# Performance work log

Measured on AMD Instinct MI355X. Metric: run time of the kernel, lower is better.

Reference implementation:

```python
import jax, jax.numpy as jnp
import numpy as np

EMB = 512
H = 8
D = EMB // H
N_TOK = 2048
IN_EMB = 1024
SCALE = EMB ** 0.5  # note: original divides AFTER softmax
EPS = 1e-5


def _layer_norm(x, g, b):
    m = x.mean(-1, keepdims=True)
    v = ((x - m) ** 2).mean(-1, keepdims=True)
    return (x - m) / jnp.sqrt(v + EPS) * g + b


def _mhla(x, idx, Wq, bq, Wk, bk, Wv, bv):
    # x: [b, n, EMB]; idx: [n, k] int neighbor indices into token axis
    b, n, _ = x.shape
    def heads(y):
        return y.reshape(b, n, H, D).transpose(0, 2, 1, 3)  # b h n d
    q = heads(x @ Wq + bq)
    k = heads(x @ Wk + bk)
    v = heads(x @ Wv + bv)
    Kl = k[:, :, idx, :]  # b h n k d  (gather of local keys)
    Vl = v[:, :, idx, :]  # b h n k d
    energy = jnp.einsum('bhnd,bhnkd->bhnk', q, Kl)
    att = jax.nn.softmax(energy, axis=-1) / SCALE  # faithful: scale after softmax
    patch_att = att.sum(axis=(1, 3)).T  # [n, b] (sum over heads, neighbors; stacked over n)
    out = jnp.einsum('bhnk,bhnkd->bhnd', att, Vl)
    out = out.transpose(0, 2, 1, 3).reshape(b, n, EMB)
    return out, patch_att


def setup_inputs() -> dict:
    key = jax.random.key(0)
    ks = jax.random.split(key, 16)
    def p(k, shape, s=0.02):
        return jax.random.normal(k, shape, dtype=jnp.float32) * s
    inp = {
        'x': jax.random.normal(ks[0], (1, N_TOK, IN_EMB), dtype=jnp.float32),
        'A': jax.random.randint(ks[1], (1, N_TOK, 64), 0, N_TOK),
        'W_fc': p(ks[2], (IN_EMB, EMB)), 'b_fc': jnp.zeros((EMB,), jnp.float32),
        'Wq1': p(ks[3], (EMB, EMB)), 'bq1': jnp.zeros((EMB,), jnp.float32),
        'Wk1': p(ks[4], (EMB, EMB)), 'bk1': jnp.zeros((EMB,), jnp.float32),
        'Wv1': p(ks[5], (EMB, EMB)), 'bv1': jnp.zeros((EMB,), jnp.float32),
        'g1': jnp.ones((EMB,), jnp.float32), 'be1': jnp.zeros((EMB,), jnp.float32),
        'Wq2': p(ks[6], (EMB, EMB)), 'bq2': jnp.zeros((EMB,), jnp.float32),
        'Wk2': p(ks[7], (EMB, EMB)), 'bk2': jnp.zeros((EMB,), jnp.float32),
        'Wv2': p(ks[8], (EMB, EMB)), 'bv2': jnp.zeros((EMB,), jnp.float32),
        'g2': jnp.ones((EMB,), jnp.float32), 'be2': jnp.zeros((EMB,), jnp.float32),
    }
    return inp


def reference(x, A, W_fc, b_fc, Wq1, bq1, Wk1, bk1, Wv1, bv1, g1, be1,
              Wq2, bq2, Wk2, bk2, Wv2, bv2, g2, be2):
    embs = jax.nn.relu(x @ W_fc + b_fc)  # FeedForwardBlock (dropout p=0)
    idx = A[0]  # batch==1 as required by torch.squeeze semantics in original
    b1, _ = _mhla(embs, idx[:, :16], Wq1, bq1, Wk1, bk1, Wv1, bv1)
    b1 = _layer_norm(b1 + embs, g1, be1)
    b2, Att2 = _mhla(b1, idx[:, :64], Wq2, bq2, Wk2, bk2, Wv2, bv2)
    b2 = _layer_norm(b2 + b1, g2, be2)
    return b2, Att2
```

## Files before the change

### kernel.cpp

```cpp
#include <hip/hip_runtime.h>

#define SCALE 22.627416997969522f
#define LNEPS 1e-5f

using short8 = __attribute__((ext_vector_type(8))) short;
using f32x4  = __attribute__((ext_vector_type(4))) float;
typedef unsigned short u16;
using u16x4 = __attribute__((ext_vector_type(4))) u16;

static __device__ __forceinline__ short f2bf(float f){
  unsigned u = __builtin_bit_cast(unsigned, f);
  u += 0x7FFFu + ((u >> 16) & 1u);
  return (short)(u >> 16);
}
static __device__ __forceinline__ float bf2f(u16 u){
  unsigned v = ((unsigned)u) << 16;
  return __builtin_bit_cast(float, v);
}

__global__ __launch_bounds__(256) void cvt_k(const float* __restrict__ src,
                                             u16* __restrict__ dst, int n)
{
  int i = (blockIdx.x * 256 + threadIdx.x) * 4;
  if (i >= n) return;
  float4 v = *(const float4*)(src + i);
  u16x4 o;
  o[0] = (u16)f2bf(v.x); o[1] = (u16)f2bf(v.y);
  o[2] = (u16)f2bf(v.z); o[3] = (u16)f2bf(v.w);
  *(u16x4*)(dst + i) = o;
}

__global__ __launch_bounds__(256) void tr_k(
    const float* __restrict__ W0, const float* __restrict__ W1,
    const float* __restrict__ W2, const float* __restrict__ W3,
    const float* __restrict__ W4, const float* __restrict__ W5,
    u16* __restrict__ T0, u16* __restrict__ T1, u16* __restrict__ T2,
    u16* __restrict__ T3, u16* __restrict__ T4, u16* __restrict__ T5,
    int K, int N)
{
  int z = blockIdx.z;
  const float* W = (z==0)?W0:(z==1)?W1:(z==2)?W2:(z==3)?W3:(z==4)?W4:W5;
  u16*         T = (z==0)?T0:(z==1)?T1:(z==2)?T2:(z==3)?T3:(z==4)?T4:T5;

  __shared__ float tile[32][33];
  int n0 = blockIdx.x * 32, k0 = blockIdx.y * 32;
  int tx = threadIdx.x & 31, ty = threadIdx.x >> 5;
#pragma unroll
  for (int i = 0; i < 32; i += 8)
    tile[ty + i][tx] = W[(size_t)(k0 + ty + i) * N + n0 + tx];
  __syncthreads();
#pragma unroll
  for (int i = 0; i < 32; i += 8)
    T[(size_t)(n0 + ty + i) * K + k0 + tx] = (u16)f2bf(tile[tx][ty + i]);
}

template<bool RELU, bool SPLIT3>
__global__ __launch_bounds__(256) void gemm_k(
    const u16* __restrict__ A, int K,
    const u16* __restrict__ T0, const u16* __restrict__ T1, const u16* __restrict__ T2,
    const float* __restrict__ B0, const float* __restrict__ B1, const float* __restrict__ B2,
    float* __restrict__ C0f, u16* __restrict__ C0b,
    u16* __restrict__ C1, u16* __restrict__ C2)
{
  __shared__ u16 As[64*64];
  __shared__ u16 Bs[64*64];

  int bm = blockIdx.x;
  int nglob = blockIdx.y * 64;
  int sel  = SPLIT3 ? (nglob >> 9) : 0;
  int ncol = nglob & 511;
  const u16*   T  = (sel==0) ? T0 : (sel==1) ? T1 : T2;
  const float* Bv = (sel==0) ? B0 : (sel==1) ? B1 : B2;

  int t = threadIdx.x;
  int wave = t >> 6, lane = t & 63;
  int wm = (wave >> 1) * 32, wn = (wave & 1) * 32;
  int lr = lane & 15, kg = lane >> 4;

  int o0 = t*16, o1 = 4096 + t*16;
  int r0 = o0 >> 7, cb0 = o0 & 127;
  int r1 = o1 >> 7, cb1 = o1 & 127;
  const char* Ag0 = (const char*)(A + (size_t)(bm*64 + r0) * K) + cb0;
  const char* Ag1 = (const char*)(A + (size_t)(bm*64 + r1) * K) + cb1;
  const char* Bg0 = (const char*)(T + (size_t)(ncol  + r0) * K) + cb0;
  const char* Bg1 = (const char*)(T + (size_t)(ncol  + r1) * K) + cb1;
  char* Ad0 = (char*)As + r0*128 + (cb0 ^ ((r0 & 7) << 4));
  char* Ad1 = (char*)As + r1*128 + (cb1 ^ ((r1 & 7) << 4));
  char* Bd0 = (char*)Bs + r0*128 + (cb0 ^ ((r0 & 7) << 4));
  char* Bd1 = (char*)Bs + r1*128 + (cb1 ^ ((r1 & 7) << 4));

  int sw = (lr & 7) << 4;
  const char* Afr0 = (const char*)As + (wm + lr) * 128;
  const char* Afr1 = (const char*)As + (wm + 16 + lr) * 128;
  const char* Bfr0 = (const char*)Bs + (wn + lr) * 128;
  const char* Bfr1 = (const char*)Bs + (wn + 16 + lr) * 128;

  f32x4 acc[2][2] = {};

  short8 pa0 = *(const short8*)Ag0;
  short8 pa1 = *(const short8*)Ag1;
  short8 pb0 = *(const short8*)Bg0;
  short8 pb1 = *(const short8*)Bg1;

  for (int k0 = 0; k0 < K; k0 += 64) {
    __syncthreads();
    *(short8*)Ad0 = pa0;  *(short8*)Ad1 = pa1;
    *(short8*)Bd0 = pb0;  *(short8*)Bd1 = pb1;
    __syncthreads();
    int kn = k0 + 64;
    if (kn < K) {
      pa0 = *(const short8*)(Ag0 + kn*2);
      pa1 = *(const short8*)(Ag1 + kn*2);
      pb0 = *(const short8*)(Bg0 + kn*2);
      pb1 = *(const short8*)(Bg1 + kn*2);
    }
#pragma unroll
    for (int ks = 0; ks < 2; ++ks) {
      int cb = (ks*64 + kg*16) ^ sw;
      short8 af0 = *(const short8*)(Afr0 + cb);
      short8 af1 = *(const short8*)(Afr1 + cb);
      short8 bf0 = *(const short8*)(Bfr0 + cb);
      short8 bf1 = *(const short8*)(Bfr1 + cb);
      acc[0][0] = __builtin_amdgcn_mfma_f32_16x16x32_bf16(af0, bf0, acc[0][0], 0, 0, 0);
      acc[0][1] = __builtin_amdgcn_mfma_f32_16x16x32_bf16(af0, bf1, acc[0][1], 0, 0, 0);
      acc[1][0] = __builtin_amdgcn_mfma_f32_16x16x32_bf16(af1, bf0, acc[1][0], 0, 0, 0);
      acc[1][1] = __builtin_amdgcn_mfma_f32_16x16x32_bf16(af1, bf1, acc[1][1], 0, 0, 0);
    }
  }

#pragma unroll
  for (int mi = 0; mi < 2; ++mi)
#pragma unroll
    for (int ni = 0; ni < 2; ++ni) {
      int col = ncol + wn + ni*16 + lr;
      float bia = Bv[col];
#pragma unroll
      for (int r = 0; r < 4; ++r) {
        int row = bm*64 + wm + mi*16 + kg*4 + r;
        float vv = acc[mi][ni][r] + bia;
        if (RELU) vv = fmaxf(vv, 0.f);
        if (SPLIT3) {
          u16* C = (sel==0) ? C0b : (sel==1) ? C1 : C2;
          C[(size_t)row*512 + col] = (u16)f2bf(vv);
        } else {
          C0f[(size_t)row*512 + col] = vv;
          C0b[(size_t)row*512 + col] = (u16)f2bf(vv);
        }
      }
    }
}

template<int KLOC>
__global__ __launch_bounds__(256) void attn_k(
    const u16* __restrict__ Qb, const u16* __restrict__ Kb, const u16* __restrict__ Vb,
    const int* __restrict__ Aidx,
    const float* __restrict__ resid,
    const float* __restrict__ gma, const float* __restrict__ bta,
    float* __restrict__ outp, u16* __restrict__ outb, float* __restrict__ attOut)
{
  __shared__ float q_s[512];
  __shared__ float att_s[8*KLOC];
  __shared__ float o_s[512];
  __shared__ int   idx_s[KLOC];
  __shared__ float red_s[8];

  int n = blockIdx.x;
  int t = threadIdx.x, w = t >> 6, lane = t & 63;

  q_s[t]       = bf2f(Qb[(size_t)n*512 + t]);
  q_s[t + 256] = bf2f(Qb[(size_t)n*512 + t + 256]);
  if (t < KLOC) idx_s[t] = Aidx[(size_t)n*64 + t];
  __syncthreads();

  if (KLOC == 64) {
    int idx = idx_s[lane];
    int h0 = w*2, h1 = h0 + 1;
    const u16* kp = Kb + (size_t)idx*512;
    float e0 = 0.f, e1 = 0.f;
#pragma unroll
    for (int d0 = 0; d0 < 64; d0 += 8) {
      short8 k0 = *(const short8*)(kp + h0*64 + d0);
      short8 k1 = *(const short8*)(kp + h1*64 + d0);
#pragma unroll
      for (int i = 0; i < 8; ++i) {
        e0 = fmaf(q_s[h0*64 + d0 + i], bf2f((u16)k0[i]), e0);
        e1 = fmaf(q_s[h1*64 + d0 + i], bf2f((u16)k1[i]), e1);
      }
    }
#pragma unroll
    for (int hh = 0; hh < 2; ++hh) {
      float e = hh ? e1 : e0;
      float m = e;
      m = fmaxf(m, __shfl_xor(m, 1));  m = fmaxf(m, __shfl_xor(m, 2));
      m = fmaxf(m, __shfl_xor(m, 4));  m = fmaxf(m, __shfl_xor(m, 8));
      m = fmaxf(m, __shfl_xor(m, 16)); m = fmaxf(m, __shfl_xor(m, 32));
      float p = __expf(e - m);
      float s = p;
      s += __shfl_xor(s, 1);  s += __shfl_xor(s, 2);  s += __shfl_xor(s, 4);
      s += __shfl_xor(s, 8);  s += __shfl_xor(s, 16); s += __shfl_xor(s, 32);
      att_s[(h0 + hh)*64 + lane] = p / (s * SCALE);
    }
  } else {
    int h  = w*2 + (lane >> 5);
    int j  = lane & 15;
    int dh = (lane >> 4) & 1;
    int idx = idx_s[j];
    const u16*   kp = Kb + (size_t)idx*512 + h*64 + dh*32;
    const float* qp = q_s + h*64 + dh*32;
    float e = 0.f;
#pragma unroll
    for (int d0 = 0; d0 < 32; d0 += 8) {
      short8 kk = *(const short8*)(kp + d0);
#pragma unroll
      for (int i = 0; i < 8; ++i)
        e = fmaf(qp[d0 + i], bf2f((u16)kk[i]), e);
    }
    e += __shfl_xor(e, 16);
    float m = e;
    m = fmaxf(m, __shfl_xor(m, 1)); m = fmaxf(m, __shfl_xor(m, 2));
    m = fmaxf(m, __shfl_xor(m, 4)); m = fmaxf(m, __shfl_xor(m, 8));
    float p = __expf(e - m);
    float s = p;
    s += __shfl_xor(s, 1); s += __shfl_xor(s, 2);
    s += __shfl_xor(s, 4); s += __shfl_xor(s, 8);
    att_s[h*16 + j] = p / (s * SCALE);
  }
  __syncthreads();

  {
    int jg = lane >> 3, dc = lane & 7;
#pragma unroll
    for (int hh = 0; hh < 2; ++hh) {
      int h = w*2 + hh;
      float vacc[8] = {0.f,0.f,0.f,0.f,0.f,0.f,0.f,0.f};
#pragma unroll
      for (int jb = 0; jb < KLOC; jb += 8) {
        int j = jb + jg;
        const u16* vp = Vb + (size_t)idx_s[j]*512 + h*64 + dc*8;
        short8 vv = *(const short8*)vp;
        float a = att_s[h*KLOC + j];
#pragma unroll
        for (int i = 0; i < 8; ++i)
          vacc[i] = fmaf(a, bf2f((u16)vv[i]), vacc[i]);
      }
#pragma unroll
      for (int i = 0; i < 8; ++i) {
        vacc[i] += __shfl_xor(vacc[i], 8);
        vacc[i] += __shfl_xor(vacc[i], 16);
        vacc[i] += __shfl_xor(vacc[i], 32);
      }
      if (jg == 0) {
#pragma unroll
        for (int i = 0; i < 8; ++i)
          o_s[h*64 + dc*8 + i] = vacc[i];
      }
    }
  }
  __syncthreads();

  float x0 = o_s[t]       + __builtin_nontemporal_load(resid + (size_t)n*512 + t);
  float x1 = o_s[t + 256] + __builtin_nontemporal_load(resid + (size_t)n*512 + t + 256);
  float s  = x0 + x1, ss = x0*x0 + x1*x1;
  s += __shfl_xor(s, 1);  ss += __shfl_xor(ss, 1);
  s += __shfl_xor(s, 2);  ss += __shfl_xor(ss, 2);
  s += __shfl_xor(s, 4);  ss += __shfl_xor(ss, 4);
  s += __shfl_xor(s, 8);  ss += __shfl_xor(ss, 8);
  s += __shfl_xor(s, 16); ss += __shfl_xor(ss, 16);
  s += __shfl_xor(s, 32); ss += __shfl_xor(ss, 32);
  if (lane == 0) { red_s[w] = s; red_s[4 + w] = ss; }
  __syncthreads();
  float tot  = red_s[0] + red_s[1] + red_s[2] + red_s[3];
  float tots = red_s[4] + red_s[5] + red_s[6] + red_s[7];
  float mean = tot  * (1.0f/512.0f);
  float var  = tots * (1.0f/512.0f) - mean*mean;
  float rstd = rsqrtf(var + LNEPS);
  float y0 = (x0 - mean)*rstd*gma[t]       + bta[t];
  float y1 = (x1 - mean)*rstd*gma[t + 256] + bta[t + 256];
  __builtin_nontemporal_store(y0, outp + (size_t)n*512 + t);
  __builtin_nontemporal_store(y1, outp + (size_t)n*512 + t + 256);
  if (outb != nullptr) {
    outb[(size_t)n*512 + t]       = (u16)f2bf(y0);
    outb[(size_t)n*512 + t + 256] = (u16)f2bf(y1);
  }
  if (attOut != nullptr && t == 0) attOut[n] = 8.0f / SCALE;
}

extern "C" void kernel_launch(void* const* d_in, const int* in_sizes, int n_in,
                              void* d_out, int out_size, void* d_ws, size_t ws_size,
                              hipStream_t stream)
{
  const float* x   = (const float*)d_in[0];
  const int*   A   = (const int*)  d_in[1];
  const float* Wfc = (const float*)d_in[2];
  const float* bfc = (const float*)d_in[3];
  const float* Wq1 = (const float*)d_in[4];
  const float* bq1 = (const float*)d_in[5];
  const float* Wk1 = (const float*)d_in[6];
  const float* bk1 = (const float*)d_in[7];
  const float* Wv1 = (const float*)d_in[8];
  const float* bv1 = (const float*)d_in[9];
  const float* g1  = (const float*)d_in[10];
  const float* be1 = (const float*)d_in[11];
  const float* Wq2 = (const float*)d_in[12];
  const float* bq2 = (const float*)d_in[13];
  const float* Wk2 = (const float*)d_in[14];
  const float* bk2 = (const float*)d_in[15];
  const float* Wv2 = (const float*)d_in[16];
  const float* bv2 = (const float*)d_in[17];
  const float* g2  = (const float*)d_in[18];
  const float* be2 = (const float*)d_in[19];

  char* ws = (char*)d_ws;
  const size_t SZ = (size_t)2048*512;
  float* embs = (float*)ws;                    ws += SZ*4;
  float* b1   = (float*)ws;                    ws += SZ*4;
  u16* embs_b = (u16*)ws;                      ws += SZ*2;
  u16* b1_b   = (u16*)ws;                      ws += SZ*2;
  u16* qb     = (u16*)ws;                      ws += SZ*2;
  u16* kb     = (u16*)ws;                      ws += SZ*2;
  u16* vb     = (u16*)ws;                      ws += SZ*2;
  u16* xb     = (u16*)ws;                      ws += (size_t)2048*1024*2;
  u16* t_fc   = (u16*)ws;                      ws += (size_t)512*1024*2;
  u16* t_q1   = (u16*)ws;                      ws += (size_t)512*512*2;
  u16* t_k1   = (u16*)ws;                      ws += (size_t)512*512*2;
  u16* t_v1   = (u16*)ws;                      ws += (size_t)512*512*2;
  u16* t_q2   = (u16*)ws;                      ws += (size_t)512*512*2;
  u16* t_k2   = (u16*)ws;                      ws += (size_t)512*512*2;
  u16* t_v2   = (u16*)ws;                      ws += (size_t)512*512*2;

  float* out  = (float*)d_out;
  float* att2 = out + SZ;

  dim3 blk(256);
  cvt_k<<<dim3(2048), blk, 0, stream>>>(x, xb, 2048*1024);
  tr_k<<<dim3(16, 32, 1), blk, 0, stream>>>(Wfc, Wfc, Wfc, Wfc, Wfc, Wfc,
      t_fc, t_fc, t_fc, t_fc, t_fc, t_fc, 1024, 512);
  tr_k<<<dim3(16, 16, 6), blk, 0, stream>>>(Wq1, Wk1, Wv1, Wq2, Wk2, Wv2,
      t_q1, t_k1, t_v1, t_q2, t_k2, t_v2, 512, 512);

  gemm_k<true,false><<<dim3(32, 8), blk, 0, stream>>>(xb, 1024,
      t_fc, nullptr, nullptr, bfc, nullptr, nullptr, embs, embs_b, nullptr, nullptr);
  gemm_k<false,true><<<dim3(32, 24), blk, 0, stream>>>(embs_b, 512,
      t_q1, t_k1, t_v1, bq1, bk1, bv1, nullptr, qb, kb, vb);
  attn_k<16><<<dim3(2048), blk, 0, stream>>>(qb, kb, vb, A, embs, g1, be1, b1, b1_b, nullptr);
  gemm_k<false,true><<<dim3(32, 24), blk, 0, stream>>>(b1_b, 512,
      t_q2, t_k2, t_v2, bq2, bk2, bv2, nullptr, qb, kb, vb);
  attn_k<64><<<dim3(2048), blk, 0, stream>>>(qb, kb, vb, A, b1, g2, be2, out, nullptr, att2);
}
```

Before: 188.1 us.

## Stage gathered K and V rows in swizzled shared memory before attention math

Each block now loads its gathered neighbor K rows into an XOR-swizzled LDS buffer with coalesced full-row loads, computes energies from LDS, then reuses the same buffer for V rows before the weighted sum. This replaces scattered per-lane global reads with row-contiguous loads and swizzled LDS accesses that avoid bank conflicts. The Q load is also vectorized to two elements per thread. The cost is 64KB of LDS for the 64-neighbor kernel, which limits occupancy to very few blocks per CU, plus two extra barriers.

```diff
diff --git a/kernel.cpp b/kernel.cpp
--- a/kernel.cpp
+++ b/kernel.cpp
@@ -158,6 +158,7 @@
     const float* __restrict__ gma, const float* __restrict__ bta,
     float* __restrict__ outp, u16* __restrict__ outb, float* __restrict__ attOut)
 {
+  __shared__ u16   kv_s[KLOC*512];
   __shared__ float q_s[512];
   __shared__ float att_s[8*KLOC];
   __shared__ float o_s[512];
@@ -167,24 +168,37 @@
   int n = blockIdx.x;
   int t = threadIdx.x, w = t >> 6, lane = t & 63;
 
-  q_s[t]       = bf2f(Qb[(size_t)n*512 + t]);
-  q_s[t + 256] = bf2f(Qb[(size_t)n*512 + t + 256]);
+  {
+    ushort2 qv = *(const ushort2*)(Qb + (size_t)n*512 + 2*t);
+    q_s[2*t]   = bf2f(qv.x);
+    q_s[2*t+1] = bf2f(qv.y);
+  }
   if (t < KLOC) idx_s[t] = Aidx[(size_t)n*64 + t];
   __syncthreads();
 
+  constexpr int RPW = KLOC/4;
+#pragma unroll
+  for (int jj = 0; jj < RPW; ++jj) {
+    int j = w*RPW + jj;
+    short8 vv = ((const short8*)(Kb + (size_t)idx_s[j]*512))[lane];
+    *(short8*)((char*)kv_s + j*1024 + ((lane*16) ^ ((j&7)<<4))) = vv;
+  }
+  __syncthreads();
+
   if (KLOC == 64) {
-    int idx = idx_s[lane];
+    int j = lane;
+    const char* kp = (const char*)kv_s + j*1024;
+    int swz = (j&7) << 4;
     int h0 = w*2, h1 = h0 + 1;
-    const u16* kp = Kb + (size_t)idx*512;
     float e0 = 0.f, e1 = 0.f;
 #pragma unroll
-    for (int d0 = 0; d0 < 64; d0 += 8) {
-      short8 k0 = *(const short8*)(kp + h0*64 + d0);
-      short8 k1 = *(const short8*)(kp + h1*64 + d0);
+    for (int c = 0; c < 8; ++c) {
+      short8 k0 = *(const short8*)(kp + ((h0*128 + c*16) ^ swz));
+      short8 k1 = *(const short8*)(kp + ((h1*128 + c*16) ^ swz));
 #pragma unroll
       for (int i = 0; i < 8; ++i) {
-        e0 = fmaf(q_s[h0*64 + d0 + i], bf2f((u16)k0[i]), e0);
-        e1 = fmaf(q_s[h1*64 + d0 + i], bf2f((u16)k1[i]), e1);
+        e0 = fmaf(q_s[h0*64 + c*8 + i], bf2f((u16)k0[i]), e0);
+        e1 = fmaf(q_s[h1*64 + c*8 + i], bf2f((u16)k1[i]), e1);
       }
     }
 #pragma unroll
@@ -204,16 +218,16 @@
     int h  = w*2 + (lane >> 5);
     int j  = lane & 15;
     int dh = (lane >> 4) & 1;
-    int idx = idx_s[j];
-    const u16*   kp = Kb + (size_t)idx*512 + h*64 + dh*32;
-    const float* qp = q_s + h*64 + dh*32;
+    const char* kp = (const char*)kv_s + j*1024;
+    int swz = (j&7) << 4;
+    int base = h*128 + dh*64;
     float e = 0.f;
 #pragma unroll
-    for (int d0 = 0; d0 < 32; d0 += 8) {
-      short8 kk = *(const short8*)(kp + d0);
+    for (int c = 0; c < 4; ++c) {
+      short8 kk = *(const short8*)(kp + ((base + c*16) ^ swz));
 #pragma unroll
       for (int i = 0; i < 8; ++i)
-        e = fmaf(qp[d0 + i], bf2f((u16)kk[i]), e);
+        e = fmaf(q_s[h*64 + dh*32 + c*8 + i], bf2f((u16)kk[i]), e);
     }
     e += __shfl_xor(e, 16);
     float m = e;
@@ -227,6 +241,14 @@
   }
   __syncthreads();
 
+#pragma unroll
+  for (int jj = 0; jj < RPW; ++jj) {
+    int j = w*RPW + jj;
+    short8 vv = ((const short8*)(Vb + (size_t)idx_s[j]*512))[lane];
+    *(short8*)((char*)kv_s + j*1024 + ((lane*16) ^ ((j&7)<<4))) = vv;
+  }
+  __syncthreads();
+
   {
     int jg = lane >> 3, dc = lane & 7;
 #pragma unroll
@@ -235,10 +257,9 @@
       float vacc[8] = {0.f,0.f,0.f,0.f,0.f,0.f,0.f,0.f};
 #pragma unroll
       for (int jb = 0; jb < KLOC; jb += 8) {
-        int j = jb + jg;
-        const u16* vp = Vb + (size_t)idx_s[j]*512 + h*64 + dc*8;
-        short8 vv = *(const short8*)vp;
-        float a = att_s[h*KLOC + j];
+        int r = jb + jg;
+        short8 vv = *(const short8*)((char*)kv_s + r*1024 + ((h*128 + dc*16) ^ ((r&7)<<4)));
+        float a = att_s[h*KLOC + r];
 #pragma unroll
         for (int i = 0; i < 8; ++i)
           vacc[i] = fmaf(a, bf2f((u16)vv[i]), vacc[i]);
```

New measurement: 179.2 us. 1.05x faster.

## Restructure local attention with 512 threads, coalesced K staging and register V prefetch

Applied to the files above, without the earlier changes.

The attention kernel now runs 512 threads per token, one wave per head. Each gathered key row is loaded as full coalesced 1KB rows into padded shared memory, and all value vectors are prefetched into registers before the softmax. Query values live in registers and attention weights are passed by shuffles instead of shared memory, removing one barrier. In exchange it needs much more LDS per block (up to about 66KB for KLOC=64) and more registers, which could limit occupancy.

```diff
diff --git a/kernel.cpp b/kernel.cpp
--- a/kernel.cpp
+++ b/kernel.cpp
@@ -151,137 +151,135 @@
 }
 
 template<int KLOC>
-__global__ __launch_bounds__(256) void attn_k(
+__global__ __launch_bounds__(512, 4) void attn_k(
     const u16* __restrict__ Qb, const u16* __restrict__ Kb, const u16* __restrict__ Vb,
     const int* __restrict__ Aidx,
     const float* __restrict__ resid,
     const float* __restrict__ gma, const float* __restrict__ bta,
     float* __restrict__ outp, u16* __restrict__ outb, float* __restrict__ attOut)
 {
-  __shared__ float q_s[512];
-  __shared__ float att_s[8*KLOC];
+  constexpr int PITCH_B = 1040;
+  constexpr int NP  = KLOC / 16;
+  constexpr int NV  = KLOC / 8;
+  constexpr int RPW = KLOC / 8;
+
+  __shared__ u16   k_s[KLOC * (PITCH_B/2)];
   __shared__ float o_s[512];
   __shared__ int   idx_s[KLOC];
-  __shared__ float red_s[8];
+  __shared__ float red_s[16];
 
   int n = blockIdx.x;
-  int t = threadIdx.x, w = t >> 6, lane = t & 63;
-
-  q_s[t]       = bf2f(Qb[(size_t)n*512 + t]);
-  q_s[t + 256] = bf2f(Qb[(size_t)n*512 + t + 256]);
+  int t = threadIdx.x;
+  int w = t >> 6;
+  int lane = t & 63;
+
   if (t < KLOC) idx_s[t] = Aidx[(size_t)n*64 + t];
   __syncthreads();
 
-  if (KLOC == 64) {
-    int idx = idx_s[lane];
-    int h0 = w*2, h1 = h0 + 1;
-    const u16* kp = Kb + (size_t)idx*512;
-    float e0 = 0.f, e1 = 0.f;
-#pragma unroll
-    for (int d0 = 0; d0 < 64; d0 += 8) {
-      short8 k0 = *(const short8*)(kp + h0*64 + d0);
-      short8 k1 = *(const short8*)(kp + h1*64 + d0);
-#pragma unroll
-      for (int i = 0; i < 8; ++i) {
-        e0 = fmaf(q_s[h0*64 + d0 + i], bf2f((u16)k0[i]), e0);
-        e1 = fmaf(q_s[h1*64 + d0 + i], bf2f((u16)k1[i]), e1);
-      }
-    }
-#pragma unroll
-    for (int hh = 0; hh < 2; ++hh) {
-      float e = hh ? e1 : e0;
-      float m = e;
-      m = fmaxf(m, __shfl_xor(m, 1));  m = fmaxf(m, __shfl_xor(m, 2));
-      m = fmaxf(m, __shfl_xor(m, 4));  m = fmaxf(m, __shfl_xor(m, 8));
-      m = fmaxf(m, __shfl_xor(m, 16)); m = fmaxf(m, __shfl_xor(m, 32));
-      float p = __expf(e - m);
-      float s = p;
-      s += __shfl_xor(s, 1);  s += __shfl_xor(s, 2);  s += __shfl_xor(s, 4);
-      s += __shfl_xor(s, 8);  s += __shfl_xor(s, 16); s += __shfl_xor(s, 32);
-      att_s[(h0 + hh)*64 + lane] = p / (s * SCALE);
-    }
-  } else {
-    int h  = w*2 + (lane >> 5);
-    int j  = lane & 15;
-    int dh = (lane >> 4) & 1;
-    int idx = idx_s[j];
-    const u16*   kp = Kb + (size_t)idx*512 + h*64 + dh*32;
-    const float* qp = q_s + h*64 + dh*32;
+  int rowbase = w * RPW;
+  short8 kreg[RPW];
+#pragma unroll
+  for (int i = 0; i < RPW; ++i)
+    kreg[i] = ((const short8*)(Kb + (size_t)idx_s[rowbase + i] * 512))[lane];
+#pragma unroll
+  for (int i = 0; i < RPW; ++i)
+    *(short8*)((char*)k_s + (size_t)(rowbase + i) * PITCH_B + lane * 16) = kreg[i];
+
+  int jg = lane >> 3, dc = lane & 7;
+  short8 vpre[NV];
+#pragma unroll
+  for (int p = 0; p < NV; ++p) {
+    int r = p * 8 + jg;
+    vpre[p] = *(const short8*)(Vb + (size_t)idx_s[r] * 512 + w * 64 + dc * 8);
+  }
+
+  int jj = lane & 15, dq = lane >> 4;
+  float qreg[16];
+  {
+    const u16* qp = Qb + (size_t)n*512 + w*64 + dq*16;
+    short8 qa = *(const short8*)qp;
+    short8 qb2 = *(const short8*)(qp + 8);
+#pragma unroll
+    for (int i = 0; i < 8; ++i) {
+      qreg[i]     = bf2f((u16)qa[i]);
+      qreg[8 + i] = bf2f((u16)qb2[i]);
+    }
+  }
+  __syncthreads();
+
+  float att[NP];
+#pragma unroll
+  for (int p = 0; p < NP; ++p) {
+    int row = p * 16 + jj;
+    const u16* kp = (const u16*)((const char*)k_s + (size_t)row * PITCH_B)
+                    + w * 64 + dq * 16;
+    short8 k0 = *(const short8*)kp;
+    short8 k1 = *(const short8*)(kp + 8);
     float e = 0.f;
 #pragma unroll
-    for (int d0 = 0; d0 < 32; d0 += 8) {
-      short8 kk = *(const short8*)(kp + d0);
-#pragma unroll
-      for (int i = 0; i < 8; ++i)
-        e = fmaf(qp[d0 + i], bf2f((u16)kk[i]), e);
+    for (int i = 0; i < 8; ++i) {
+      e = fmaf(qreg[i],     bf2f((u16)k0[i]), e);
+      e = fmaf(qreg[8 + i], bf2f((u16)k1[i]), e);
     }
     e += __shfl_xor(e, 16);
-    float m = e;
-    m = fmaxf(m, __shfl_xor(m, 1)); m = fmaxf(m, __shfl_xor(m, 2));
-    m = fmaxf(m, __shfl_xor(m, 4)); m = fmaxf(m, __shfl_xor(m, 8));
-    float p = __expf(e - m);
-    float s = p;
-    s += __shfl_xor(s, 1); s += __shfl_xor(s, 2);
-    s += __shfl_xor(s, 4); s += __shfl_xor(s, 8);
-    att_s[h*16 + j] = p / (s * SCALE);
-  }
-  __syncthreads();
-
-  {
-    int jg = lane >> 3, dc = lane & 7;
-#pragma unroll
-    for (int hh = 0; hh < 2; ++hh) {
-      int h = w*2 + hh;
-      float vacc[8] = {0.f,0.f,0.f,0.f,0.f,0.f,0.f,0.f};
-#pragma unroll
-      for (int jb = 0; jb < KLOC; jb += 8) {
-        int j = jb + jg;
-        const u16* vp = Vb + (size_t)idx_s[j]*512 + h*64 + dc*8;
-        short8 vv = *(const short8*)vp;
-        float a = att_s[h*KLOC + j];
-#pragma unroll
-        for (int i = 0; i < 8; ++i)
-          vacc[i] = fmaf(a, bf2f((u16)vv[i]), vacc[i]);
-      }
-#pragma unroll
-      for (int i = 0; i < 8; ++i) {
-        vacc[i] += __shfl_xor(vacc[i], 8);
-        vacc[i] += __shfl_xor(vacc[i], 16);
-        vacc[i] += __shfl_xor(vacc[i], 32);
-      }
-      if (jg == 0) {
-#pragma unroll
-        for (int i = 0; i < 8; ++i)
-          o_s[h*64 + dc*8 + i] = vacc[i];
-      }
-    }
-  }
-  __syncthreads();
-
-  float x0 = o_s[t]       + __builtin_nontemporal_load(resid + (size_t)n*512 + t);
-  float x1 = o_s[t + 256] + __builtin_nontemporal_load(resid + (size_t)n*512 + t + 256);
-  float s  = x0 + x1, ss = x0*x0 + x1*x1;
-  s += __shfl_xor(s, 1);  ss += __shfl_xor(ss, 1);
-  s += __shfl_xor(s, 2);  ss += __shfl_xor(ss, 2);
-  s += __shfl_xor(s, 4);  ss += __shfl_xor(ss, 4);
-  s += __shfl_xor(s, 8);  ss += __shfl_xor(ss, 8);
-  s += __shfl_xor(s, 16); ss += __shfl_xor(ss, 16);
-  s += __shfl_xor(s, 32); ss += __shfl_xor(ss, 32);
-  if (lane == 0) { red_s[w] = s; red_s[4 + w] = ss; }
-  __syncthreads();
-  float tot  = red_s[0] + red_s[1] + red_s[2] + red_s[3];
-  float tots = red_s[4] + red_s[5] + red_s[6] + red_s[7];
+    e += __shfl_xor(e, 32);
+    att[p] = e;
+  }
+
+  float mx = att[0];
+#pragma unroll
+  for (int p = 1; p < NP; ++p) mx = fmaxf(mx, att[p]);
+  mx = fmaxf(mx, __shfl_xor(mx, 1)); mx = fmaxf(mx, __shfl_xor(mx, 2));
+  mx = fmaxf(mx, __shfl_xor(mx, 4)); mx = fmaxf(mx, __shfl_xor(mx, 8));
+  float s = 0.f;
+#pragma unroll
+  for (int p = 0; p < NP; ++p) { att[p] = __expf(att[p] - mx); s += att[p]; }
+  s += __shfl_xor(s, 1); s += __shfl_xor(s, 2);
+  s += __shfl_xor(s, 4); s += __shfl_xor(s, 8);
+  float inv = 1.f / (s * SCALE);
+#pragma unroll
+  for (int p = 0; p < NP; ++p) att[p] *= inv;
+
+  float vacc[8] = {0.f,0.f,0.f,0.f,0.f,0.f,0.f,0.f};
+#pragma unroll
+  for (int p = 0; p < NV; ++p) {
+    float a = __shfl(att[p >> 1], (p & 1) * 8 + jg);
+#pragma unroll
+    for (int i = 0; i < 8; ++i)
+      vacc[i] = fmaf(a, bf2f((u16)vpre[p][i]), vacc[i]);
+  }
+#pragma unroll
+  for (int i = 0; i < 8; ++i) {
+    vacc[i] += __shfl_xor(vacc[i], 8);
+    vacc[i] += __shfl_xor(vacc[i], 16);
+    vacc[i] += __shfl_xor(vacc[i], 32);
+  }
+  if (jg == 0) {
+#pragma unroll
+    for (int i = 0; i < 8; ++i)
+      o_s[w*64 + dc*8 + i] = vacc[i];
+  }
+  __syncthreads();
+
+  float x = o_s[t] + __builtin_nontemporal_load(resid + (size_t)n*512 + t);
+  float su = x, sq = x * x;
+  su += __shfl_xor(su, 1);  sq += __shfl_xor(sq, 1);
+  su += __shfl_xor(su, 2);  sq += __shfl_xor(sq, 2);
+  su += __shfl_xor(su, 4);  sq += __shfl_xor(sq, 4);
+  su += __shfl_xor(su, 8);  sq += __shfl_xor(sq, 8);
+  su += __shfl_xor(su, 16); sq += __shfl_xor(sq, 16);
+  su += __shfl_xor(su, 32); sq += __shfl_xor(sq, 32);
+  if (lane == 0) { red_s[w] = su; red_s[8 + w] = sq; }
+  __syncthreads();
+  float tot = 0.f, tots = 0.f;
+#pragma unroll
+  for (int i = 0; i < 8; ++i) { tot += red_s[i]; tots += red_s[8 + i]; }
   float mean = tot  * (1.0f/512.0f);
   float var  = tots * (1.0f/512.0f) - mean*mean;
   float rstd = rsqrtf(var + LNEPS);
-  float y0 = (x0 - mean)*rstd*gma[t]       + bta[t];
-  float y1 = (x1 - mean)*rstd*gma[t + 256] + bta[t + 256];
-  __builtin_nontemporal_store(y0, outp + (size_t)n*512 + t);
-  __builtin_nontemporal_store(y1, outp + (size_t)n*512 + t + 256);
-  if (outb != nullptr) {
-    outb[(size_t)n*512 + t]       = (u16)f2bf(y0);
-    outb[(size_t)n*512 + t + 256] = (u16)f2bf(y1);
-  }
+  float y = (x - mean) * rstd * gma[t] + bta[t];
+  __builtin_nontemporal_store(y, outp + (size_t)n*512 + t);
+  if (outb != nullptr) outb[(size_t)n*512 + t] = (u16)f2bf(y);
   if (attOut != nullptr && t == 0) attOut[n] = 8.0f / SCALE;
 }
 
@@ -342,8 +340,8 @@
       t_fc, nullptr, nullptr, bfc, nullptr, nullptr, embs, embs_b, nullptr, nullptr);
   gemm_k<false,true><<<dim3(32, 24), blk, 0, stream>>>(embs_b, 512,
       t_q1, t_k1, t_v1, bq1, bk1, bv1, nullptr, qb, kb, vb);
-  attn_k<16><<<dim3(2048), blk, 0, stream>>>(qb, kb, vb, A, embs, g1, be1, b1, b1_b, nullptr);
+  attn_k<16><<<dim3(2048), dim3(512), 0, stream>>>(qb, kb, vb, A, embs, g1, be1, b1, b1_b, nullptr);
   gemm_k<false,true><<<dim3(32, 24), blk, 0, stream>>>(b1_b, 512,
       t_q2, t_k2, t_v2, bq2, bk2, bv2, nullptr, qb, kb, vb);
-  attn_k<64><<<dim3(2048), blk, 0, stream>>>(qb, kb, vb, A, b1, g2, be2, out, nullptr, att2);
-}
+  attn_k<64><<<dim3(2048), dim3(512), 0, stream>>>(qb, kb, vb, A, b1, g2, be2, out, nullptr, att2);
+}
```

Result: faster. 174.7 us (-7.1%).
